# Optimization experiments

Hardware: AMD Instinct MI355X
Metric: run time of the kernel (lower is better)

The kernel has to match this reference:

```python
import jax, jax.numpy as jnp
import numpy as np

B, T, E, H = 4, 1024, 768, 12
HD = E // H                      # 64
R = 2                            # lora rank
LORA_SCALE = 1.0 / R             # loralib default lora_alpha=1 -> alpha/r
NUM_BUCKETS, MAX_DIST = 320, 800


def _rel_bucket(rel):
    nb = NUM_BUCKETS // 2                      # 160
    buckets = (rel > 0).astype(jnp.int32) * nb
    rel = jnp.abs(rel)
    max_exact = nb // 2                        # 80
    is_small = rel < max_exact
    log_ratio = jnp.log(jnp.maximum(rel, 1).astype(jnp.float32) / max_exact)
    large = max_exact + (log_ratio / np.log(MAX_DIST / max_exact) * (nb - max_exact)).astype(jnp.int32)
    large = jnp.minimum(large, nb - 1)
    return buckets + jnp.where(is_small, rel, large)


def setup_inputs() -> dict:
    key = jax.random.key(0)
    ks = jax.random.split(key, 22)
    s = 0.02
    w = lambda k, shape: jax.random.normal(k, shape, jnp.float32) * s
    return {
        "hidden_states": jax.random.normal(ks[0], (B, T, E), jnp.float32),
        "Wq": w(ks[1], (E, E)), "bq": w(ks[2], (E,)),
        "Wk": w(ks[3], (E, E)), "bk": w(ks[4], (E,)),
        "Wv": w(ks[5], (E, E)), "bv": w(ks[6], (E,)),
        "Aq": w(ks[7], (R, E)), "Bq": w(ks[8], (E, R)),
        "Ak": w(ks[9], (R, E)), "Bk": w(ks[10], (E, R)),
        "Av": w(ks[11], (R, E)), "Bv": w(ks[12], (E, R)),
        "Wo": w(ks[13], (E, E)), "bo": w(ks[14], (E,)),
        "Wg": w(ks[15], (8, HD)), "bg": w(ks[16], (8,)),
        "gru_const": jnp.ones((1, H, 1, 1), jnp.float32),
        "rel_embed": w(ks[17], (NUM_BUCKETS, H)),
    }


def reference(hidden_states, Wq, bq, Wk, bk, Wv, bv,
              Aq, Bq, Ak, Bk, Av, Bv, Wo, bo, Wg, bg, gru_const, rel_embed):
    Bsz, Tq, _ = hidden_states.shape
    # --- relative position bias [H, T, T] ---
    pos = jnp.arange(Tq)
    bucket = _rel_bucket(pos[None, :] - pos[:, None])
    pos_bias = rel_embed[bucket].transpose(2, 0, 1)
    # --- dynamic gate from hidden states, per head/position ---
    g = hidden_states.reshape(Bsz, Tq, H, HD).transpose(0, 2, 1, 3)      # [B,H,T,hd]
    gp = jnp.einsum('bhtd,ed->bhte', g, Wg) + bg                          # [B,H,T,8]
    gp = gp.reshape(Bsz, H, Tq, 2, 4).sum(-1)                             # [B,H,T,2]
    gates = jax.nn.sigmoid(gp)
    gate_a, gate_b = gates[..., :1], gates[..., 1:]
    gate = gate_a * (gate_b * gru_const - 1.0) + 2.0                      # [B,H,T,1]
    gated_bias = gate * pos_bias[None]                                    # [B,H,T,T]
    # --- projections: original double-applies q/k/v_proj (proj+LoRA, then
    #     again inside F.multi_head_attention_forward via separate proj weights) ---
    lin = lambda x, W, b: jnp.einsum('bte,oe->bto', x, W) + b
    lora = lambda x, A, Bm: jnp.einsum('bte,re,or->bto', x, A, Bm) * LORA_SCALE
    x = hidden_states
    q1 = lin(x, Wq, bq) + lora(x, Aq, Bq)
    k1 = lin(x, Wk, bk) + lora(x, Ak, Bk)
    v1 = lin(x, Wv, bv) + lora(x, Av, Bv)
    q = lin(q1, Wq, bq) * (HD ** -0.5)
    k = lin(k1, Wk, bk)
    v = lin(v1, Wv, bv)
    qh = q.reshape(Bsz, Tq, H, HD).transpose(0, 2, 1, 3)
    kh = k.reshape(Bsz, Tq, H, HD).transpose(0, 2, 1, 3)
    vh = v.reshape(Bsz, Tq, H, HD).transpose(0, 2, 1, 3)
    scores = jnp.einsum('bhqd,bhkd->bhqk', qh, kh) + gated_bias
    attn = jax.nn.softmax(scores, axis=-1)
    ctx = jnp.einsum('bhqk,bhkd->bhqd', attn, vh)
    out = ctx.transpose(0, 2, 1, 3).reshape(Bsz, Tq, E)
    return jnp.einsum('bte,oe->bto', out, Wo) + bo
```

## Files before the change

kernel.cpp:

```cpp
#include <hip/hip_runtime.h>
#include <math.h>

#define TT 1024
#define EE 768
#define HH 12

typedef __attribute__((ext_vector_type(8))) __bf16 bf16x8;
typedef __attribute__((ext_vector_type(4))) float f32x4;

__device__ __forceinline__ unsigned short f2b(float f) {
    unsigned int u = __float_as_uint(f);
    unsigned int r = (u + 0x7fffu + ((u >> 16) & 1u)) >> 16;
    return (unsigned short)r;
}

#define GLD16(gsrc, ldst) \
    __builtin_amdgcn_global_load_lds( \
        (const __attribute__((address_space(1))) unsigned int*)(gsrc), \
        (__attribute__((address_space(3))) unsigned int*)(ldst), 16, 0, 0)

__global__ __launch_bounds__(256)
void prep_k(const float* __restrict__ hs, const float* __restrict__ Wq,
            const float* __restrict__ Wk, const float* __restrict__ Wv,
            const float* __restrict__ Wo, unsigned short* __restrict__ out) {
    size_t i = 4 * (size_t)(blockIdx.x * 256 + threadIdx.x);
    if (i >= 5505024) return;
    const float* src;
    if (i < 3145728)      src = hs + i;
    else if (i < 3735552) src = Wq + (i - 3145728);
    else if (i < 4325376) src = Wk + (i - 3735552);
    else if (i < 4915200) src = Wv + (i - 4325376);
    else                  src = Wo + (i - 4915200);
    float4 f = *(const float4*)src;
    unsigned int lo = (unsigned int)f2b(f.x) | ((unsigned int)f2b(f.y) << 16);
    unsigned int hi = (unsigned int)f2b(f.z) | ((unsigned int)f2b(f.w) << 16);
    uint2 p; p.x = lo; p.y = hi;
    *(uint2*)&out[i] = p;
}

__global__ __launch_bounds__(256)
void wT_k(const float* __restrict__ Wq, const float* __restrict__ Wk,
          const float* __restrict__ Wv, unsigned short* __restrict__ WT_all) {
    __shared__ unsigned short Ts[128 * 136];
    const int v = blockIdx.x;
    const int mat = v / 36, tile = v % 36;
    const int tr = tile / 6, tc = tile % 6;
    const float* S = mat == 0 ? Wq : (mat == 1 ? Wk : Wv);
    const int tid = threadIdx.x;
    #pragma unroll
    for (int i = 0; i < 16; ++i) {
        int idx = i * 256 + tid;
        int row = idx >> 5, col4 = (idx & 31) * 4;
        float4 f = *(const float4*)&S[(size_t)(tr * 128 + row) * EE + tc * 128 + col4];
        Ts[(col4 + 0) * 136 + row] = f2b(f.x);
        Ts[(col4 + 1) * 136 + row] = f2b(f.y);
        Ts[(col4 + 2) * 136 + row] = f2b(f.z);
        Ts[(col4 + 3) * 136 + row] = f2b(f.w);
    }
    __syncthreads();
    unsigned short* dst = WT_all + (size_t)mat * 589824;
    #pragma unroll
    for (int i = 0; i < 8; ++i) {
        int idx = i * 256 + tid;
        int rr = idx >> 4, cg = (idx & 15) * 8;
        *(uint4*)&dst[(size_t)(tc * 128 + rr) * EE + tr * 128 + cg] =
            *(const uint4*)&Ts[rr * 136 + cg];
    }
}

__global__ void biastab_k(const float* __restrict__ rel_embed,
                          float* __restrict__ biasTab) {
    int idx = blockIdx.x * 256 + threadIdx.x;
    if (idx >= 2047 * 12) return;
    int h = idx % 12;
    int rr = idx / 12;
    int rel = rr - 1023;
    int base = rel > 0 ? 160 : 0;
    int ar = rel < 0 ? -rel : rel;
    int bkt;
    if (ar < 80) {
        bkt = base + ar;
    } else {
        double lr = log((double)ar / 80.0);
        int large = 80 + (int)(lr / log(10.0) * 80.0);
        if (large > 159) large = 159;
        bkt = base + large;
    }
    biasTab[h * 2048 + rr] = rel_embed[bkt * 12 + h];
}

__global__ __launch_bounds__(256)
void gates_k(const float* __restrict__ hs, const float* __restrict__ Wg,
             const float* __restrict__ bg, const float* __restrict__ gru,
             float* __restrict__ gate) {
    __shared__ float WgS[8][64];
    __shared__ float bgS[8];
    __shared__ float gcS[12];
    const int tid = threadIdx.x;
    for (int i = tid; i < 512; i += 256) WgS[i >> 6][i & 63] = Wg[i];
    if (tid < 8)  bgS[tid] = bg[tid];
    if (tid < 12) gcS[tid] = gru[tid];
    __syncthreads();
    int idx = blockIdx.x * 256 + tid;
    int t = idx & 1023;
    int h = (idx >> 10) % 12;
    int b = idx / (12 * 1024);
    const float* gp = hs + ((size_t)(b * TT + t)) * EE + h * 64;
    float acc[8];
    #pragma unroll
    for (int e = 0; e < 8; ++e) acc[e] = 0.f;
    #pragma unroll
    for (int d4 = 0; d4 < 64; d4 += 4) {
        float4 u = *(const float4*)(gp + d4);
        float gv[4] = {u.x, u.y, u.z, u.w};
        #pragma unroll
        for (int j = 0; j < 4; ++j) {
            #pragma unroll
            for (int e = 0; e < 8; ++e) acc[e] += gv[j] * WgS[e][d4 + j];
        }
    }
    float s0 = acc[0] + acc[1] + acc[2] + acc[3] + bgS[0] + bgS[1] + bgS[2] + bgS[3];
    float s1 = acc[4] + acc[5] + acc[6] + acc[7] + bgS[4] + bgS[5] + bgS[6] + bgS[7];
    float ga = 1.f / (1.f + __expf(-s0));
    float gb = 1.f / (1.f + __expf(-s1));
    gate[idx] = ga * (gb * gcS[h] - 1.0f) + 2.0f;
}

__global__ __launch_bounds__(64)
void lora_down_k(const float* __restrict__ x,
                 const float* __restrict__ Aq, const float* __restrict__ Ak,
                 const float* __restrict__ Av, float* __restrict__ xA) {
    const int m = blockIdx.x;
    const int lane = threadIdx.x;
    const float* xp = x + (size_t)m * EE;
    float s[6] = {0.f, 0.f, 0.f, 0.f, 0.f, 0.f};
    for (int c = lane * 4; c < EE; c += 256) {
        float4 u = *(const float4*)(xp + c);
        float xv[4] = {u.x, u.y, u.z, u.w};
        #pragma unroll
        for (int j = 0; j < 4; ++j) {
            int e = c + j;
            s[0] += xv[j] * Aq[e];       s[1] += xv[j] * Aq[EE + e];
            s[2] += xv[j] * Ak[e];       s[3] += xv[j] * Ak[EE + e];
            s[4] += xv[j] * Av[e];       s[5] += xv[j] * Av[EE + e];
        }
    }
    #pragma unroll
    for (int off = 32; off > 0; off >>= 1) {
        #pragma unroll
        for (int i = 0; i < 6; ++i) s[i] += __shfl_down(s[i], off, 64);
    }
    if (lane == 0) {
        xA[m * 2 + 0] = s[0];                xA[m * 2 + 1] = s[1];
        xA[8192 + m * 2 + 0] = s[2];         xA[8192 + m * 2 + 1] = s[3];
        xA[16384 + m * 2 + 0] = s[4];        xA[16384 + m * 2 + 1] = s[5];
    }
}

__global__ __launch_bounds__(256)
void bias2_k(const float* __restrict__ Wq, const float* __restrict__ Wk,
             const float* __restrict__ Wv,
             const float* __restrict__ bq, const float* __restrict__ bk,
             const float* __restrict__ bv,
             const float* __restrict__ Bq, const float* __restrict__ Bk,
             const float* __restrict__ Bv,
             float* __restrict__ bias2, float* __restrict__ B2) {
    __shared__ float bvS[768];
    __shared__ float BmS[1536];
    const int tid = threadIdx.x;
    int v = blockIdx.x;
    int sel = v / 4, nb = (v % 4) * 192;
    const float* W = sel == 0 ? Wq : (sel == 1 ? Wk : Wv);
    const float* bvec = sel == 0 ? bq : (sel == 1 ? bk : bv);
    const float* Bm = sel == 0 ? Bq : (sel == 1 ? Bk : Bv);
    for (int i = tid; i < 768; i += 256) bvS[i] = bvec[i];
    for (int i = tid; i < 1536; i += 256) BmS[i] = Bm[i];
    __syncthreads();
    if (tid < 192) {
        int n = nb + tid;
        const float* Wrow = W + (size_t)n * EE;
        float a0 = 0.f, a1 = 0.f, a2 = 0.f;
        for (int o = 0; o < EE; o += 4) {
            float4 w = *(const float4*)&Wrow[o];
            a0 += w.x * bvS[o] + w.y * bvS[o + 1] + w.z * bvS[o + 2] + w.w * bvS[o + 3];
            a1 += w.x * BmS[o * 2] + w.y * BmS[o * 2 + 2] + w.z * BmS[o * 2 + 4] + w.w * BmS[o * 2 + 6];
            a2 += w.x * BmS[o * 2 + 1] + w.y * BmS[o * 2 + 3] + w.z * BmS[o * 2 + 5] + w.w * BmS[o * 2 + 7];
        }
        bias2[sel * 768 + n] = a0 + bvS[n];
        B2[sel * 1536 + n * 2 + 0] = a1;
        B2[sel * 1536 + n * 2 + 1] = a2;
    }
}

__global__ __launch_bounds__(256, 2)
void wgemm_k(const unsigned short* __restrict__ Wall_b,
             const unsigned short* __restrict__ WT_all,
             unsigned short* __restrict__ W2_all) {
    __shared__ unsigned short At[128 * 32];
    __shared__ unsigned short Bt[128 * 32];
    const int tid = threadIdx.x;
    const int bxx = blockIdx.x;
    const int sel = bxx / 36, tile = bxx % 36;
    const int row0 = (tile / 6) * 128, col0 = (tile % 6) * 128;
    const unsigned short* A = Wall_b + (size_t)sel * 589824;
    const unsigned short* Bw = WT_all + (size_t)sel * 589824;

    const int lane = tid & 63, wv = tid >> 6;
    const int wm = (wv & 1) * 64, wn = (wv >> 1) * 64;
    const int l15 = lane & 15, g8 = (lane >> 4) * 8;
    const int lr = lane >> 2, lc = (lane & 3) * 8;
    const int c0 = wv * 2, c1 = wv * 2 + 1;
    const unsigned short* Abase0 = A + (size_t)(row0 + c0 * 16 + lr) * EE + lc;
    const unsigned short* Abase1 = A + (size_t)(row0 + c1 * 16 + lr) * EE + lc;
    const unsigned short* Bbase0 = Bw + (size_t)(col0 + c0 * 16 + lr) * EE + lc;
    const unsigned short* Bbase1 = Bw + (size_t)(col0 + c1 * 16 + lr) * EE + lc;

    f32x4 zero4 = {0.f, 0.f, 0.f, 0.f};
    f32x4 acc[4][4];
    #pragma unroll
    for (int i = 0; i < 4; ++i)
        #pragma unroll
        for (int j = 0; j < 4; ++j) acc[i][j] = zero4;

    for (int kt = 0; kt < 768; kt += 32) {
        GLD16(Abase0 + kt, &At[c0 * 512]);
        GLD16(Abase1 + kt, &At[c1 * 512]);
        GLD16(Bbase0 + kt, &Bt[c0 * 512]);
        GLD16(Bbase1 + kt, &Bt[c1 * 512]);
        __syncthreads();
        bf16x8 af[4], bf[4];
        #pragma unroll
        for (int mt = 0; mt < 4; ++mt) af[mt] = *(const bf16x8*)&At[(wm + mt * 16 + l15) * 32 + g8];
        #pragma unroll
        for (int nt = 0; nt < 4; ++nt) bf[nt] = *(const bf16x8*)&Bt[(wn + nt * 16 + l15) * 32 + g8];
        #pragma unroll
        for (int mt = 0; mt < 4; ++mt)
            #pragma unroll
            for (int nt = 0; nt < 4; ++nt)
                acc[mt][nt] = __builtin_amdgcn_mfma_f32_16x16x32_bf16(af[mt], bf[nt], acc[mt][nt], 0, 0, 0);
        __syncthreads();
    }
    unsigned short* out = W2_all + (size_t)sel * 589824;
    const int g4 = (lane >> 4) * 4;
    #pragma unroll
    for (int mt = 0; mt < 4; ++mt)
        #pragma unroll
        for (int r = 0; r < 4; ++r) {
            int grow = row0 + wm + mt * 16 + g4 + r;
            #pragma unroll
            for (int nt = 0; nt < 4; ++nt) {
                int ncol = col0 + wn + nt * 16 + l15;
                out[(size_t)grow * EE + ncol] = f2b(acc[mt][nt][r]);
            }
        }
}

__global__ __launch_bounds__(256, 2)
void qkv_gemm_k(const unsigned short* __restrict__ Aall,
                const unsigned short* __restrict__ W2_all,
                const float* __restrict__ bias2,
                const float* __restrict__ xA, const float* __restrict__ B2,
                unsigned short* __restrict__ qb, unsigned short* __restrict__ kb,
                unsigned short* __restrict__ vb) {
    __shared__ unsigned short At[128 * 32];
    __shared__ unsigned short Bt[128 * 32];
    const int tid = threadIdx.x;
    const int bx = blockIdx.x, by = blockIdx.y;
    const int sel = bx / 6;
    const int col0 = (bx % 6) * 128, row0 = by * 128;
    const unsigned short* Wb = W2_all + (size_t)sel * 589824;
    const float* bias = bias2 + sel * 768;
    const float scale = (sel == 0) ? 0.125f : 1.0f;

    const int lane = tid & 63, wv = tid >> 6;
    const int wm = (wv & 1) * 64, wn = (wv >> 1) * 64;
    const int l15 = lane & 15, g8 = (lane >> 4) * 8;
    const int lr = lane >> 2, lc = (lane & 3) * 8;
    const int c0 = wv * 2, c1 = wv * 2 + 1;
    const unsigned short* Abase0 = Aall + (size_t)(row0 + c0 * 16 + lr) * EE + lc;
    const unsigned short* Abase1 = Aall + (size_t)(row0 + c1 * 16 + lr) * EE + lc;
    const unsigned short* Bbase0 = Wb + (size_t)(col0 + c0 * 16 + lr) * EE + lc;
    const unsigned short* Bbase1 = Wb + (size_t)(col0 + c1 * 16 + lr) * EE + lc;

    f32x4 zero4 = {0.f, 0.f, 0.f, 0.f};
    f32x4 acc[4][4];
    #pragma unroll
    for (int i = 0; i < 4; ++i)
        #pragma unroll
        for (int j = 0; j < 4; ++j) acc[i][j] = zero4;

    for (int kt = 0; kt < 768; kt += 32) {
        GLD16(Abase0 + kt, &At[c0 * 512]);
        GLD16(Abase1 + kt, &At[c1 * 512]);
        GLD16(Bbase0 + kt, &Bt[c0 * 512]);
        GLD16(Bbase1 + kt, &Bt[c1 * 512]);
        __syncthreads();
        bf16x8 af[4], bf[4];
        #pragma unroll
        for (int mt = 0; mt < 4; ++mt) af[mt] = *(const bf16x8*)&At[(wm + mt * 16 + l15) * 32 + g8];
        #pragma unroll
        for (int nt = 0; nt < 4; ++nt) bf[nt] = *(const bf16x8*)&Bt[(wn + nt * 16 + l15) * 32 + g8];
        #pragma unroll
        for (int mt = 0; mt < 4; ++mt)
            #pragma unroll
            for (int nt = 0; nt < 4; ++nt)
                acc[mt][nt] = __builtin_amdgcn_mfma_f32_16x16x32_bf16(af[mt], bf[nt], acc[mt][nt], 0, 0, 0);
        __syncthreads();
    }

    unsigned short* dst = sel == 0 ? qb : (sel == 1 ? kb : vb);
    const float* Lbase = xA + sel * 8192;
    const float* B2s   = B2 + sel * 1536;
    const int g4 = (lane >> 4) * 4;
    #pragma unroll
    for (int mt = 0; mt < 4; ++mt) {
        #pragma unroll
        for (int r = 0; r < 4; ++r) {
            size_t grow = (size_t)row0 + wm + mt * 16 + g4 + r;
            float l0 = Lbase[grow * 2], l1 = Lbase[grow * 2 + 1];
            #pragma unroll
            for (int nt = 0; nt < 4; ++nt) {
                int ncol = col0 + wn + nt * 16 + l15;
                float c = (acc[mt][nt][r] + bias[ncol]
                           + 0.5f * (l0 * B2s[ncol * 2] + l1 * B2s[ncol * 2 + 1])) * scale;
                dst[grow * EE + ncol] = f2b(c);
            }
        }
    }
}

__global__ __launch_bounds__(256)
void vT_k(const unsigned short* __restrict__ vb, unsigned short* __restrict__ Vtg) {
    __shared__ unsigned short Vs[64 * 72];
    const int tid = threadIdx.x;
    const int tt = blockIdx.x, h = blockIdx.y, b = blockIdx.z;
    const int r = tid >> 3, cc = (tid & 7) * 8;
    #pragma unroll
    for (int i = 0; i < 2; ++i) {
        int row = i * 32 + r;
        const unsigned short* vp = vb + (size_t)(b * TT + tt * 64 + row) * EE + h * 64 + cc;
        *(uint4*)&Vs[row * 72 + cc] = *(const uint4*)vp;
    }
    __syncthreads();
    #pragma unroll
    for (int i = 0; i < 2; ++i) {
        int d = i * 32 + r;
        unsigned short tmp[8] __attribute__((aligned(16)));
        #pragma unroll
        for (int j = 0; j < 8; ++j) tmp[j] = Vs[(cc + j) * 72 + d];
        *(uint4*)&Vtg[((size_t)(b * HH + h) * 64 + d) * TT + tt * 64 + cc] = *(const uint4*)tmp;
    }
}

__global__ __launch_bounds__(256, 3)
void attn_k(const unsigned short* __restrict__ qb, const unsigned short* __restrict__ kb,
            const unsigned short* __restrict__ Vtg, const float* __restrict__ gate,
            const float* __restrict__ biasTab, unsigned short* __restrict__ ctx) {
    __shared__ unsigned short Qs[64 * 72];
    __shared__ unsigned short Ks[64 * 72];
    __shared__ unsigned short Vt[64 * 72];
    __shared__ unsigned short Ps[64 * 72];
    __shared__ float btabS[2048];
    const int tid = threadIdx.x;
    const int qt = blockIdx.x, h = blockIdx.y, b = blockIdx.z;

    for (int i = tid; i < 2047; i += 256) btabS[i] = biasTab[h * 2048 + i];

    const int srow = tid >> 2, scol = (tid & 3) * 16;
    {
        const unsigned short* qp = qb + ((size_t)(b * TT + qt * 64 + srow)) * EE + h * 64 + scol;
        *(uint4*)&Qs[srow * 72 + scol]     = *(const uint4*)qp;
        *(uint4*)&Qs[srow * 72 + scol + 8] = *(const uint4*)(qp + 8);
    }
    const int lane = tid & 63, wv = tid >> 6;
    const int m0 = wv * 16;
    const int l15 = lane & 15, g = lane >> 4;

    float li[4];
    f32x4 zero4 = {0.f, 0.f, 0.f, 0.f};
    f32x4 oa[4];
    #pragma unroll
    for (int r = 0; r < 4; ++r) li[r] = 0.f;
    #pragma unroll
    for (int nt = 0; nt < 4; ++nt) oa[nt] = zero4;
    float gv[4];
    #pragma unroll
    for (int r = 0; r < 4; ++r)
        gv[r] = gate[((size_t)(b * HH + h)) * TT + qt * 64 + m0 + 4 * g + r];
    const unsigned short* vrow = Vtg + ((size_t)(b * HH + h) * 64 + srow) * TT;
    __syncthreads();

    for (int kt = 0; kt < 16; ++kt) {
        {
            const unsigned short* kp = kb + ((size_t)(b * TT + kt * 64 + srow)) * EE + h * 64 + scol;
            *(uint4*)&Ks[srow * 72 + scol]     = *(const uint4*)kp;
            *(uint4*)&Ks[srow * 72 + scol + 8] = *(const uint4*)(kp + 8);
            const unsigned short* vp = vrow + kt * 64 + scol;
            *(uint4*)&Vt[srow * 72 + scol]     = *(const uint4*)vp;
            *(uint4*)&Vt[srow * 72 + scol + 8] = *(const uint4*)(vp + 8);
        }
        __syncthreads();
        f32x4 sa[4];
        #pragma unroll
        for (int nt = 0; nt < 4; ++nt) sa[nt] = zero4;
        bf16x8 aq0 = *(const bf16x8*)&Qs[(m0 + l15) * 72 + g * 8];
        bf16x8 aq1 = *(const bf16x8*)&Qs[(m0 + l15) * 72 + 32 + g * 8];
        #pragma unroll
        for (int nt = 0; nt < 4; ++nt) {
            bf16x8 bk0 = *(const bf16x8*)&Ks[(nt * 16 + l15) * 72 + g * 8];
            bf16x8 bk1 = *(const bf16x8*)&Ks[(nt * 16 + l15) * 72 + 32 + g * 8];
            sa[nt] = __builtin_amdgcn_mfma_f32_16x16x32_bf16(aq0, bk0, sa[nt], 0, 0, 0);
            sa[nt] = __builtin_amdgcn_mfma_f32_16x16x32_bf16(aq1, bk1, sa[nt], 0, 0, 0);
        }
        #pragma unroll
        for (int nt = 0; nt < 4; ++nt) {
            int ibase = kt * 64 + nt * 16 + l15 + 1023 - qt * 64 - m0 - 4 * g;
            #pragma unroll
            for (int r = 0; r < 4; ++r) {
                float e = __expf(sa[nt][r] + gv[r] * btabS[ibase - r]);
                li[r] += e;
                Ps[(m0 + 4 * g + r) * 72 + nt * 16 + l15] = f2b(e);
            }
        }
        bf16x8 ap0 = *(const bf16x8*)&Ps[(m0 + l15) * 72 + g * 8];
        bf16x8 ap1 = *(const bf16x8*)&Ps[(m0 + l15) * 72 + 32 + g * 8];
        #pragma unroll
        for (int nt = 0; nt < 4; ++nt) {
            bf16x8 bv0 = *(const bf16x8*)&Vt[(nt * 16 + l15) * 72 + g * 8];
            bf16x8 bv1 = *(const bf16x8*)&Vt[(nt * 16 + l15) * 72 + 32 + g * 8];
            oa[nt] = __builtin_amdgcn_mfma_f32_16x16x32_bf16(ap0, bv0, oa[nt], 0, 0, 0);
            oa[nt] = __builtin_amdgcn_mfma_f32_16x16x32_bf16(ap1, bv1, oa[nt], 0, 0, 0);
        }
        __syncthreads();
    }
    #pragma unroll
    for (int r = 0; r < 4; ++r) {
        #pragma unroll
        for (int msk = 1; msk < 16; msk <<= 1)
            li[r] += __shfl_xor(li[r], msk, 16);
    }
    #pragma unroll
    for (int nt = 0; nt < 4; ++nt)
        #pragma unroll
        for (int r = 0; r < 4; ++r)
            Ks[(m0 + 4 * g + r) * 72 + nt * 16 + l15] = f2b(oa[nt][r] / li[r]);
    __syncthreads();
    {
        unsigned short* cp = ctx + ((size_t)(b * TT + qt * 64 + srow)) * EE + h * 64 + scol;
        *(uint4*)cp       = *(const uint4*)&Ks[srow * 72 + scol];
        *(uint4*)(cp + 8) = *(const uint4*)&Ks[srow * 72 + scol + 8];
    }
}

__global__ __launch_bounds__(256, 2)
void out_gemm_k(const unsigned short* __restrict__ Aall,
                const unsigned short* __restrict__ Wob,
                const float* __restrict__ bo, float* __restrict__ outf) {
    __shared__ unsigned short At[128 * 32];
    __shared__ unsigned short Bt[128 * 32];
    const int tid = threadIdx.x;
    const int col0 = blockIdx.x * 128, row0 = blockIdx.y * 128;

    const int lane = tid & 63, wv = tid >> 6;
    const int wm = (wv & 1) * 64, wn = (wv >> 1) * 64;
    const int l15 = lane & 15, g8 = (lane >> 4) * 8;
    const int lr = lane >> 2, lc = (lane & 3) * 8;
    const int c0 = wv * 2, c1 = wv * 2 + 1;
    const unsigned short* Abase0 = Aall + (size_t)(row0 + c0 * 16 + lr) * EE + lc;
    const unsigned short* Abase1 = Aall + (size_t)(row0 + c1 * 16 + lr) * EE + lc;
    const unsigned short* Bbase0 = Wob + (size_t)(col0 + c0 * 16 + lr) * EE + lc;
    const unsigned short* Bbase1 = Wob + (size_t)(col0 + c1 * 16 + lr) * EE + lc;

    f32x4 zero4 = {0.f, 0.f, 0.f, 0.f};
    f32x4 acc[4][4];
    #pragma unroll
    for (int i = 0; i < 4; ++i)
        #pragma unroll
        for (int j = 0; j < 4; ++j) acc[i][j] = zero4;

    for (int kt = 0; kt < 768; kt += 32) {
        GLD16(Abase0 + kt, &At[c0 * 512]);
        GLD16(Abase1 + kt, &At[c1 * 512]);
        GLD16(Bbase0 + kt, &Bt[c0 * 512]);
        GLD16(Bbase1 + kt, &Bt[c1 * 512]);
        __syncthreads();
        bf16x8 af[4], bf[4];
        #pragma unroll
        for (int mt = 0; mt < 4; ++mt) af[mt] = *(const bf16x8*)&At[(wm + mt * 16 + l15) * 32 + g8];
        #pragma unroll
        for (int nt = 0; nt < 4; ++nt) bf[nt] = *(const bf16x8*)&Bt[(wn + nt * 16 + l15) * 32 + g8];
        #pragma unroll
        for (int mt = 0; mt < 4; ++mt)
            #pragma unroll
            for (int nt = 0; nt < 4; ++nt)
                acc[mt][nt] = __builtin_amdgcn_mfma_f32_16x16x32_bf16(af[mt], bf[nt], acc[mt][nt], 0, 0, 0);
        __syncthreads();
    }
    const int g4 = (lane >> 4) * 4;
    #pragma unroll
    for (int mt = 0; mt < 4; ++mt)
        #pragma unroll
        for (int r = 0; r < 4; ++r) {
            size_t grow = (size_t)row0 + wm + mt * 16 + g4 + r;
            #pragma unroll
            for (int nt = 0; nt < 4; ++nt) {
                int ncol = col0 + wn + nt * 16 + l15;
                outf[grow * EE + ncol] = acc[mt][nt][r] + bo[ncol];
            }
        }
}

extern "C" void kernel_launch(void* const* d_in, const int* in_sizes, int n_in,
                              void* d_out, int out_size, void* d_ws, size_t ws_size,
                              hipStream_t stream) {
    const float* hs  = (const float*)d_in[0];
    const float* Wq  = (const float*)d_in[1];
    const float* bq  = (const float*)d_in[2];
    const float* Wk  = (const float*)d_in[3];
    const float* bk  = (const float*)d_in[4];
    const float* Wv  = (const float*)d_in[5];
    const float* bv  = (const float*)d_in[6];
    const float* Aq  = (const float*)d_in[7];
    const float* Bq  = (const float*)d_in[8];
    const float* Ak  = (const float*)d_in[9];
    const float* Bk  = (const float*)d_in[10];
    const float* Av  = (const float*)d_in[11];
    const float* Bv  = (const float*)d_in[12];
    const float* Wo  = (const float*)d_in[13];
    const float* bo  = (const float*)d_in[14];
    const float* Wg  = (const float*)d_in[15];
    const float* bg  = (const float*)d_in[16];
    const float* gru = (const float*)d_in[17];
    const float* rel = (const float*)d_in[18];

    float* ws = (float*)d_ws;
    float* gate    = ws;
    float* biasTab = gate + 49152;
    float* xA      = biasTab + 24576;
    float* bias2   = xA + 24576;
    float* B2      = bias2 + 2304;
    unsigned short* hsb    = (unsigned short*)(B2 + 4608);
    unsigned short* Wall_b = hsb + 3145728;
    unsigned short* WT_all = Wall_b + 4 * 589824;
    unsigned short* W2_all = WT_all + 3 * 589824;
    unsigned short* qb     = W2_all + 3 * 589824;
    unsigned short* kb     = qb + 3145728;
    unsigned short* vb     = kb + 3145728;
    unsigned short* Vtg    = vb + 3145728;
    unsigned short* ctxb   = Vtg + 3145728;

    prep_k<<<5376, 256, 0, stream>>>(hs, Wq, Wk, Wv, Wo, hsb);
    wT_k<<<108, 256, 0, stream>>>(Wq, Wk, Wv, WT_all);
    gates_k<<<192, 256, 0, stream>>>(hs, Wg, bg, gru, gate);
    lora_down_k<<<4096, 64, 0, stream>>>(hs, Aq, Ak, Av, xA);
    biastab_k<<<96, 256, 0, stream>>>(rel, biasTab);
    bias2_k<<<12, 256, 0, stream>>>(Wq, Wk, Wv, bq, bk, bv, Bq, Bk, Bv, bias2, B2);

    wgemm_k<<<108, 256, 0, stream>>>(Wall_b, WT_all, W2_all);
    qkv_gemm_k<<<dim3(18, 32), 256, 0, stream>>>(hsb, W2_all, bias2, xA, B2, qb, kb, vb);
    vT_k<<<dim3(16, 12, 4), 256, 0, stream>>>(vb, Vtg);
    attn_k<<<dim3(16, 12, 4), 256, 0, stream>>>(qb, kb, Vtg, gate, biasTab, ctxb);
    out_gemm_k<<<dim3(6, 32), 256, 0, stream>>>(ctxb, Wall_b + 3 * 589824, bo, (float*)d_out);
}
```

Measured before the change: 260.6 us.

## Merge setup kernels, fuse hs reads, prefetch K/V in attention, raise occupancy

Six preprocessing launches become two. One block-partitioned kernel handles weight casts, the W transpose, the bias table and bias2. The other reads each 16-row slab of hidden states once to produce the bf16 copy, the gates and the LoRA down-projection. The q scale of 0.125 moves from the qkv GEMM epilogue into W2 and bias2. The attention kernel now prefetches the next K/V tile into registers while the current tile is computed, and the GEMM launch bounds change from 2 to 3 blocks per SM. This cuts launch overhead and redundant hs traffic, at the cost of more register pressure and a possible drop in occupancy in the fused kernels.

```diff
diff --git a/kernel.cpp b/kernel.cpp
--- a/kernel.cpp
+++ b/kernel.cpp
@@ -20,179 +20,196 @@
         (__attribute__((address_space(3))) unsigned int*)(ldst), 16, 0, 0)
 
 __global__ __launch_bounds__(256)
-void prep_k(const float* __restrict__ hs, const float* __restrict__ Wq,
-            const float* __restrict__ Wk, const float* __restrict__ Wv,
-            const float* __restrict__ Wo, unsigned short* __restrict__ out) {
-    size_t i = 4 * (size_t)(blockIdx.x * 256 + threadIdx.x);
-    if (i >= 5505024) return;
-    const float* src;
-    if (i < 3145728)      src = hs + i;
-    else if (i < 3735552) src = Wq + (i - 3145728);
-    else if (i < 4325376) src = Wk + (i - 3735552);
-    else if (i < 4915200) src = Wv + (i - 4325376);
-    else                  src = Wo + (i - 4915200);
-    float4 f = *(const float4*)src;
-    unsigned int lo = (unsigned int)f2b(f.x) | ((unsigned int)f2b(f.y) << 16);
-    unsigned int hi = (unsigned int)f2b(f.z) | ((unsigned int)f2b(f.w) << 16);
-    uint2 p; p.x = lo; p.y = hi;
-    *(uint2*)&out[i] = p;
+void setupA_k(const float* __restrict__ Wq, const float* __restrict__ Wk,
+              const float* __restrict__ Wv, const float* __restrict__ Wo,
+              const float* __restrict__ bq, const float* __restrict__ bk,
+              const float* __restrict__ bv,
+              const float* __restrict__ Bq, const float* __restrict__ Bk,
+              const float* __restrict__ Bv, const float* __restrict__ rel,
+              unsigned short* __restrict__ Wall_b, unsigned short* __restrict__ WT_all,
+              float* __restrict__ biasTab, float* __restrict__ bias2,
+              float* __restrict__ B2) {
+    __shared__ __align__(16) char smem[34816];
+    const int bid = blockIdx.x, tid = threadIdx.x;
+
+    if (bid < 1152) {
+        size_t base = (size_t)bid * 2048 + tid * 8;
+        int mat = (int)(base / 589824);
+        size_t local = base % 589824;
+        const float* S = mat == 0 ? Wq : (mat == 1 ? Wk : (mat == 2 ? Wv : Wo));
+        float4 a = *(const float4*)&S[local];
+        float4 c = *(const float4*)&S[local + 4];
+        unsigned short hb[8] __attribute__((aligned(16)));
+        hb[0] = f2b(a.x); hb[1] = f2b(a.y); hb[2] = f2b(a.z); hb[3] = f2b(a.w);
+        hb[4] = f2b(c.x); hb[5] = f2b(c.y); hb[6] = f2b(c.z); hb[7] = f2b(c.w);
+        *(uint4*)&Wall_b[base] = *(const uint4*)hb;
+    } else if (bid < 1260) {
+        unsigned short* Ts = (unsigned short*)smem;
+        int v = bid - 1152;
+        int mat = v / 36, tile = v % 36;
+        int tr = tile / 6, tc = tile % 6;
+        const float* S = mat == 0 ? Wq : (mat == 1 ? Wk : Wv);
+        #pragma unroll
+        for (int i = 0; i < 16; ++i) {
+            int idx = i * 256 + tid;
+            int row = idx >> 5, col4 = (idx & 31) * 4;
+            float4 f = *(const float4*)&S[(size_t)(tr * 128 + row) * EE + tc * 128 + col4];
+            Ts[(col4 + 0) * 136 + row] = f2b(f.x);
+            Ts[(col4 + 1) * 136 + row] = f2b(f.y);
+            Ts[(col4 + 2) * 136 + row] = f2b(f.z);
+            Ts[(col4 + 3) * 136 + row] = f2b(f.w);
+        }
+        __syncthreads();
+        unsigned short* dst = WT_all + (size_t)mat * 589824;
+        #pragma unroll
+        for (int i = 0; i < 8; ++i) {
+            int idx = i * 256 + tid;
+            int rr = idx >> 4, cg = (idx & 15) * 8;
+            *(uint4*)&dst[(size_t)(tc * 128 + rr) * EE + tr * 128 + cg] =
+                *(const uint4*)&Ts[rr * 136 + cg];
+        }
+    } else if (bid < 1356) {
+        int idx = (bid - 1260) * 256 + tid;
+        if (idx < 2047 * 12) {
+            int h = idx % 12;
+            int rr = idx / 12;
+            int relv = rr - 1023;
+            int base = relv > 0 ? 160 : 0;
+            int ar = relv < 0 ? -relv : relv;
+            int bkt;
+            if (ar < 80) bkt = base + ar;
+            else {
+                double lr = log((double)ar / 80.0);
+                int large = 80 + (int)(lr / log(10.0) * 80.0);
+                if (large > 159) large = 159;
+                bkt = base + large;
+            }
+            biasTab[h * 2048 + rr] = rel[bkt * 12 + h];
+        }
+    } else {
+        float* bvS = (float*)smem;
+        float* BmS = bvS + 768;
+        int v = bid - 1356;
+        int sel = v / 4, nb = (v % 4) * 192;
+        const float* W = sel == 0 ? Wq : (sel == 1 ? Wk : Wv);
+        const float* bvec = sel == 0 ? bq : (sel == 1 ? bk : bv);
+        const float* Bm = sel == 0 ? Bq : (sel == 1 ? Bk : Bv);
+        for (int i = tid; i < 768; i += 256) bvS[i] = bvec[i];
+        for (int i = tid; i < 1536; i += 256) BmS[i] = Bm[i];
+        __syncthreads();
+        if (tid < 192) {
+            int n = nb + tid;
+            const float* Wrow = W + (size_t)n * EE;
+            float a0 = 0.f, a1 = 0.f, a2 = 0.f;
+            for (int o = 0; o < EE; o += 4) {
+                float4 w = *(const float4*)&Wrow[o];
+                a0 += w.x * bvS[o] + w.y * bvS[o + 1] + w.z * bvS[o + 2] + w.w * bvS[o + 3];
+                a1 += w.x * BmS[o * 2] + w.y * BmS[o * 2 + 2] + w.z * BmS[o * 2 + 4] + w.w * BmS[o * 2 + 6];
+                a2 += w.x * BmS[o * 2 + 1] + w.y * BmS[o * 2 + 3] + w.z * BmS[o * 2 + 5] + w.w * BmS[o * 2 + 7];
+            }
+            float sc = (sel == 0) ? 0.125f : 1.0f;
+            bias2[sel * 768 + n] = (a0 + bvS[n]) * sc;
+            B2[sel * 1536 + n * 2 + 0] = a1 * sc;
+            B2[sel * 1536 + n * 2 + 1] = a2 * sc;
+        }
+    }
 }
 
 __global__ __launch_bounds__(256)
-void wT_k(const float* __restrict__ Wq, const float* __restrict__ Wk,
-          const float* __restrict__ Wv, unsigned short* __restrict__ WT_all) {
-    __shared__ unsigned short Ts[128 * 136];
-    const int v = blockIdx.x;
-    const int mat = v / 36, tile = v % 36;
-    const int tr = tile / 6, tc = tile % 6;
-    const float* S = mat == 0 ? Wq : (mat == 1 ? Wk : Wv);
-    const int tid = threadIdx.x;
-    #pragma unroll
-    for (int i = 0; i < 16; ++i) {
-        int idx = i * 256 + tid;
-        int row = idx >> 5, col4 = (idx & 31) * 4;
-        float4 f = *(const float4*)&S[(size_t)(tr * 128 + row) * EE + tc * 128 + col4];
-        Ts[(col4 + 0) * 136 + row] = f2b(f.x);
-        Ts[(col4 + 1) * 136 + row] = f2b(f.y);
-        Ts[(col4 + 2) * 136 + row] = f2b(f.z);
-        Ts[(col4 + 3) * 136 + row] = f2b(f.w);
-    }
-    __syncthreads();
-    unsigned short* dst = WT_all + (size_t)mat * 589824;
-    #pragma unroll
-    for (int i = 0; i < 8; ++i) {
-        int idx = i * 256 + tid;
-        int rr = idx >> 4, cg = (idx & 15) * 8;
-        *(uint4*)&dst[(size_t)(tc * 128 + rr) * EE + tr * 128 + cg] =
-            *(const uint4*)&Ts[rr * 136 + cg];
-    }
-}
-
-__global__ void biastab_k(const float* __restrict__ rel_embed,
-                          float* __restrict__ biasTab) {
-    int idx = blockIdx.x * 256 + threadIdx.x;
-    if (idx >= 2047 * 12) return;
-    int h = idx % 12;
-    int rr = idx / 12;
-    int rel = rr - 1023;
-    int base = rel > 0 ? 160 : 0;
-    int ar = rel < 0 ? -rel : rel;
-    int bkt;
-    if (ar < 80) {
-        bkt = base + ar;
-    } else {
-        double lr = log((double)ar / 80.0);
-        int large = 80 + (int)(lr / log(10.0) * 80.0);
-        if (large > 159) large = 159;
-        bkt = base + large;
-    }
-    biasTab[h * 2048 + rr] = rel_embed[bkt * 12 + h];
-}
-
-__global__ __launch_bounds__(256)
-void gates_k(const float* __restrict__ hs, const float* __restrict__ Wg,
-             const float* __restrict__ bg, const float* __restrict__ gru,
-             float* __restrict__ gate) {
-    __shared__ float WgS[8][64];
+void setupB_k(const float* __restrict__ hs, const float* __restrict__ Wg,
+              const float* __restrict__ bg, const float* __restrict__ gru,
+              const float* __restrict__ Aq, const float* __restrict__ Ak,
+              const float* __restrict__ Av,
+              unsigned short* __restrict__ hsb, float* __restrict__ gate,
+              float* __restrict__ xA) {
+    __shared__ float rowF[16 * 772];
+    __shared__ float AS[6 * 768];
+    __shared__ float WgS[8 * 68];
+    __shared__ float gpS[16 * 100];
+    __shared__ float redS[4 * 96];
     __shared__ float bgS[8];
     __shared__ float gcS[12];
     const int tid = threadIdx.x;
-    for (int i = tid; i < 512; i += 256) WgS[i >> 6][i & 63] = Wg[i];
+    const int m0 = blockIdx.x * 16;
+
+    for (int i = tid; i < 512; i += 256) WgS[(i >> 6) * 68 + (i & 63)] = Wg[i];
+    for (int i = tid; i < 1152; i += 256) {
+        int which = i / 192, c4 = (i % 192) * 4;
+        const float* src = (which < 2 ? Aq : (which < 4 ? Ak : Av)) + (which & 1) * 768 + c4;
+        float4 f = *(const float4*)src;
+        AS[which * 768 + c4 + 0] = f.x; AS[which * 768 + c4 + 1] = f.y;
+        AS[which * 768 + c4 + 2] = f.z; AS[which * 768 + c4 + 3] = f.w;
+    }
     if (tid < 8)  bgS[tid] = bg[tid];
     if (tid < 12) gcS[tid] = gru[tid];
+    #pragma unroll
+    for (int i = 0; i < 12; ++i) {
+        int idx = i * 256 + tid;
+        int row = idx / 192, c4 = (idx % 192) * 4;
+        float4 f = *(const float4*)&hs[(size_t)(m0 + row) * EE + c4];
+        rowF[row * 772 + c4 + 0] = f.x; rowF[row * 772 + c4 + 1] = f.y;
+        rowF[row * 772 + c4 + 2] = f.z; rowF[row * 772 + c4 + 3] = f.w;
+        unsigned int lo = (unsigned int)f2b(f.x) | ((unsigned int)f2b(f.y) << 16);
+        unsigned int hi = (unsigned int)f2b(f.z) | ((unsigned int)f2b(f.w) << 16);
+        uint2 p; p.x = lo; p.y = hi;
+        *(uint2*)&hsb[(size_t)(m0 + row) * EE + c4] = p;
+    }
     __syncthreads();
-    int idx = blockIdx.x * 256 + tid;
-    int t = idx & 1023;
-    int h = (idx >> 10) % 12;
-    int b = idx / (12 * 1024);
-    const float* gp = hs + ((size_t)(b * TT + t)) * EE + h * 64;
-    float acc[8];
-    #pragma unroll
-    for (int e = 0; e < 8; ++e) acc[e] = 0.f;
-    #pragma unroll
-    for (int d4 = 0; d4 < 64; d4 += 4) {
-        float4 u = *(const float4*)(gp + d4);
-        float gv[4] = {u.x, u.y, u.z, u.w};
-        #pragma unroll
-        for (int j = 0; j < 4; ++j) {
-            #pragma unroll
-            for (int e = 0; e < 8; ++e) acc[e] += gv[j] * WgS[e][d4 + j];
-        }
-    }
-    float s0 = acc[0] + acc[1] + acc[2] + acc[3] + bgS[0] + bgS[1] + bgS[2] + bgS[3];
-    float s1 = acc[4] + acc[5] + acc[6] + acc[7] + bgS[4] + bgS[5] + bgS[6] + bgS[7];
-    float ga = 1.f / (1.f + __expf(-s0));
-    float gb = 1.f / (1.f + __expf(-s1));
-    gate[idx] = ga * (gb * gcS[h] - 1.0f) + 2.0f;
-}
-
-__global__ __launch_bounds__(64)
-void lora_down_k(const float* __restrict__ x,
-                 const float* __restrict__ Aq, const float* __restrict__ Ak,
-                 const float* __restrict__ Av, float* __restrict__ xA) {
-    const int m = blockIdx.x;
-    const int lane = threadIdx.x;
-    const float* xp = x + (size_t)m * EE;
-    float s[6] = {0.f, 0.f, 0.f, 0.f, 0.f, 0.f};
-    for (int c = lane * 4; c < EE; c += 256) {
-        float4 u = *(const float4*)(xp + c);
-        float xv[4] = {u.x, u.y, u.z, u.w};
-        #pragma unroll
-        for (int j = 0; j < 4; ++j) {
-            int e = c + j;
-            s[0] += xv[j] * Aq[e];       s[1] += xv[j] * Aq[EE + e];
-            s[2] += xv[j] * Ak[e];       s[3] += xv[j] * Ak[EE + e];
-            s[4] += xv[j] * Av[e];       s[5] += xv[j] * Av[EE + e];
-        }
-    }
-    #pragma unroll
-    for (int off = 32; off > 0; off >>= 1) {
-        #pragma unroll
-        for (int i = 0; i < 6; ++i) s[i] += __shfl_down(s[i], off, 64);
-    }
-    if (lane == 0) {
-        xA[m * 2 + 0] = s[0];                xA[m * 2 + 1] = s[1];
-        xA[8192 + m * 2 + 0] = s[2];         xA[8192 + m * 2 + 1] = s[3];
-        xA[16384 + m * 2 + 0] = s[4];        xA[16384 + m * 2 + 1] = s[5];
-    }
-}
-
-__global__ __launch_bounds__(256)
-void bias2_k(const float* __restrict__ Wq, const float* __restrict__ Wk,
-             const float* __restrict__ Wv,
-             const float* __restrict__ bq, const float* __restrict__ bk,
-             const float* __restrict__ bv,
-             const float* __restrict__ Bq, const float* __restrict__ Bk,
-             const float* __restrict__ Bv,
-             float* __restrict__ bias2, float* __restrict__ B2) {
-    __shared__ float bvS[768];
-    __shared__ float BmS[1536];
-    const int tid = threadIdx.x;
-    int v = blockIdx.x;
-    int sel = v / 4, nb = (v % 4) * 192;
-    const float* W = sel == 0 ? Wq : (sel == 1 ? Wk : Wv);
-    const float* bvec = sel == 0 ? bq : (sel == 1 ? bk : bv);
-    const float* Bm = sel == 0 ? Bq : (sel == 1 ? Bk : Bv);
-    for (int i = tid; i < 768; i += 256) bvS[i] = bvec[i];
-    for (int i = tid; i < 1536; i += 256) BmS[i] = Bm[i];
+    #pragma unroll
+    for (int j = 0; j < 6; ++j) {
+        int idx = j * 256 + tid;
+        int row = idx & 15, q = idx >> 4;
+        int h = q % 12, e = q / 12;
+        const float* rp = &rowF[row * 772 + h * 64];
+        const float* wp = &WgS[e * 68];
+        float a = 0.f;
+        #pragma unroll 16
+        for (int d = 0; d < 64; ++d) a += rp[d] * wp[d];
+        gpS[row * 100 + h * 8 + e] = a;
+    }
+    {
+        int row = tid & 15, seg = tid >> 4;
+        float s[6] = {0.f, 0.f, 0.f, 0.f, 0.f, 0.f};
+        #pragma unroll 8
+        for (int j = 0; j < 48; ++j) {
+            int e = seg * 48 + j;
+            float xv = rowF[row * 772 + e];
+            s[0] += xv * AS[e];            s[1] += xv * AS[768 + e];
+            s[2] += xv * AS[1536 + e];     s[3] += xv * AS[2304 + e];
+            s[4] += xv * AS[3072 + e];     s[5] += xv * AS[3840 + e];
+        }
+        #pragma unroll
+        for (int i = 0; i < 6; ++i) {
+            s[i] += __shfl_xor(s[i], 16, 64);
+            s[i] += __shfl_xor(s[i], 32, 64);
+        }
+        int lane = tid & 63, w = tid >> 6;
+        if ((lane >> 4) == 0)
+            #pragma unroll
+            for (int i = 0; i < 6; ++i) redS[w * 96 + row * 6 + i] = s[i];
+    }
     __syncthreads();
+    if (tid < 96) {
+        int row = tid / 6, i = tid % 6;
+        float v = redS[row * 6 + i] + redS[96 + row * 6 + i] +
+                  redS[192 + row * 6 + i] + redS[288 + row * 6 + i];
+        int sel = i >> 1, r = i & 1;
+        xA[sel * 8192 + (size_t)(m0 + row) * 2 + r] = v;
+    }
     if (tid < 192) {
-        int n = nb + tid;
-        const float* Wrow = W + (size_t)n * EE;
-        float a0 = 0.f, a1 = 0.f, a2 = 0.f;
-        for (int o = 0; o < EE; o += 4) {
-            float4 w = *(const float4*)&Wrow[o];
-            a0 += w.x * bvS[o] + w.y * bvS[o + 1] + w.z * bvS[o + 2] + w.w * bvS[o + 3];
-            a1 += w.x * BmS[o * 2] + w.y * BmS[o * 2 + 2] + w.z * BmS[o * 2 + 4] + w.w * BmS[o * 2 + 6];
-            a2 += w.x * BmS[o * 2 + 1] + w.y * BmS[o * 2 + 3] + w.z * BmS[o * 2 + 5] + w.w * BmS[o * 2 + 7];
-        }
-        bias2[sel * 768 + n] = a0 + bvS[n];
-        B2[sel * 1536 + n * 2 + 0] = a1;
-        B2[sel * 1536 + n * 2 + 1] = a2;
-    }
-}
-
-__global__ __launch_bounds__(256, 2)
+        int row = tid / 12, h = tid % 12;
+        const float* gp = &gpS[row * 100 + h * 8];
+        float s0 = gp[0] + gp[1] + gp[2] + gp[3] + bgS[0] + bgS[1] + bgS[2] + bgS[3];
+        float s1 = gp[4] + gp[5] + gp[6] + gp[7] + bgS[4] + bgS[5] + bgS[6] + bgS[7];
+        float ga = 1.f / (1.f + __expf(-s0));
+        float gb = 1.f / (1.f + __expf(-s1));
+        int m = m0 + row;
+        int b = m >> 10, tp = m & 1023;
+        gate[((size_t)b * HH + h) * TT + tp] = ga * (gb * gcS[h] - 1.0f) + 2.0f;
+    }
+}
+
+__global__ __launch_bounds__(256, 3)
 void wgemm_k(const unsigned short* __restrict__ Wall_b,
              const unsigned short* __restrict__ WT_all,
              unsigned short* __restrict__ W2_all) {
@@ -241,6 +258,7 @@
         __syncthreads();
     }
     unsigned short* out = W2_all + (size_t)sel * 589824;
+    const float sc = (sel == 0) ? 0.125f : 1.0f;
     const int g4 = (lane >> 4) * 4;
     #pragma unroll
     for (int mt = 0; mt < 4; ++mt)
@@ -250,12 +268,12 @@
             #pragma unroll
             for (int nt = 0; nt < 4; ++nt) {
                 int ncol = col0 + wn + nt * 16 + l15;
-                out[(size_t)grow * EE + ncol] = f2b(acc[mt][nt][r]);
+                out[(size_t)grow * EE + ncol] = f2b(acc[mt][nt][r] * sc);
             }
         }
 }
 
-__global__ __launch_bounds__(256, 2)
+__global__ __launch_bounds__(256, 3)
 void qkv_gemm_k(const unsigned short* __restrict__ Aall,
                 const unsigned short* __restrict__ W2_all,
                 const float* __restrict__ bias2,
@@ -270,7 +288,6 @@
     const int col0 = (bx % 6) * 128, row0 = by * 128;
     const unsigned short* Wb = W2_all + (size_t)sel * 589824;
     const float* bias = bias2 + sel * 768;
-    const float scale = (sel == 0) ? 0.125f : 1.0f;
 
     const int lane = tid & 63, wv = tid >> 6;
     const int wm = (wv & 1) * 64, wn = (wv >> 1) * 64;
@@ -321,8 +338,8 @@
             #pragma unroll
             for (int nt = 0; nt < 4; ++nt) {
                 int ncol = col0 + wn + nt * 16 + l15;
-                float c = (acc[mt][nt][r] + bias[ncol]
-                           + 0.5f * (l0 * B2s[ncol * 2] + l1 * B2s[ncol * 2 + 1])) * scale;
+                float c = acc[mt][nt][r] + bias[ncol]
+                          + 0.5f * (l0 * B2s[ncol * 2] + l1 * B2s[ncol * 2 + 1]);
                 dst[grow * EE + ncol] = f2b(c);
             }
         }
@@ -387,19 +404,30 @@
     #pragma unroll
     for (int r = 0; r < 4; ++r)
         gv[r] = gate[((size_t)(b * HH + h)) * TT + qt * 64 + m0 + 4 * g + r];
-    const unsigned short* vrow = Vtg + ((size_t)(b * HH + h) * 64 + srow) * TT;
-    __syncthreads();
+
+    const unsigned short* kpbase = kb + ((size_t)(b * TT + srow)) * EE + h * 64 + scol;
+    const unsigned short* vpbase = Vtg + ((size_t)(b * HH + h) * 64 + srow) * TT + scol;
+
+    uint4 kr0 = *(const uint4*)kpbase;
+    uint4 kr1 = *(const uint4*)(kpbase + 8);
+    uint4 vr0 = *(const uint4*)vpbase;
+    uint4 vr1 = *(const uint4*)(vpbase + 8);
 
     for (int kt = 0; kt < 16; ++kt) {
-        {
-            const unsigned short* kp = kb + ((size_t)(b * TT + kt * 64 + srow)) * EE + h * 64 + scol;
-            *(uint4*)&Ks[srow * 72 + scol]     = *(const uint4*)kp;
-            *(uint4*)&Ks[srow * 72 + scol + 8] = *(const uint4*)(kp + 8);
-            const unsigned short* vp = vrow + kt * 64 + scol;
-            *(uint4*)&Vt[srow * 72 + scol]     = *(const uint4*)vp;
-            *(uint4*)&Vt[srow * 72 + scol + 8] = *(const uint4*)(vp + 8);
-        }
-        __syncthreads();
+        __syncthreads();
+        *(uint4*)&Ks[srow * 72 + scol]     = kr0;
+        *(uint4*)&Ks[srow * 72 + scol + 8] = kr1;
+        *(uint4*)&Vt[srow * 72 + scol]     = vr0;
+        *(uint4*)&Vt[srow * 72 + scol + 8] = vr1;
+        __syncthreads();
+        if (kt < 15) {
+            const unsigned short* kp = kpbase + (size_t)(kt + 1) * 64 * EE;
+            kr0 = *(const uint4*)kp;
+            kr1 = *(const uint4*)(kp + 8);
+            const unsigned short* vp = vpbase + (kt + 1) * 64;
+            vr0 = *(const uint4*)vp;
+            vr1 = *(const uint4*)(vp + 8);
+        }
         f32x4 sa[4];
         #pragma unroll
         for (int nt = 0; nt < 4; ++nt) sa[nt] = zero4;
@@ -431,8 +459,8 @@
             oa[nt] = __builtin_amdgcn_mfma_f32_16x16x32_bf16(ap0, bv0, oa[nt], 0, 0, 0);
             oa[nt] = __builtin_amdgcn_mfma_f32_16x16x32_bf16(ap1, bv1, oa[nt], 0, 0, 0);
         }
-        __syncthreads();
-    }
+    }
+    __syncthreads();
     #pragma unroll
     for (int r = 0; r < 4; ++r) {
         #pragma unroll
@@ -452,7 +480,7 @@
     }
 }
 
-__global__ __launch_bounds__(256, 2)
+__global__ __launch_bounds__(256, 3)
 void out_gemm_k(const unsigned short* __restrict__ Aall,
                 const unsigned short* __restrict__ Wob,
                 const float* __restrict__ bo, float* __restrict__ outf) {
@@ -549,13 +577,9 @@
     unsigned short* Vtg    = vb + 3145728;
     unsigned short* ctxb   = Vtg + 3145728;
 
-    prep_k<<<5376, 256, 0, stream>>>(hs, Wq, Wk, Wv, Wo, hsb);
-    wT_k<<<108, 256, 0, stream>>>(Wq, Wk, Wv, WT_all);
-    gates_k<<<192, 256, 0, stream>>>(hs, Wg, bg, gru, gate);
-    lora_down_k<<<4096, 64, 0, stream>>>(hs, Aq, Ak, Av, xA);
-    biastab_k<<<96, 256, 0, stream>>>(rel, biasTab);
-    bias2_k<<<12, 256, 0, stream>>>(Wq, Wk, Wv, bq, bk, bv, Bq, Bk, Bv, bias2, B2);
-
+    setupA_k<<<1368, 256, 0, stream>>>(Wq, Wk, Wv, Wo, bq, bk, bv, Bq, Bk, Bv, rel,
+                                       Wall_b, WT_all, biasTab, bias2, B2);
+    setupB_k<<<256, 256, 0, stream>>>(hs, Wg, bg, gru, Aq, Ak, Av, hsb, gate, xA);
     wgemm_k<<<108, 256, 0, stream>>>(Wall_b, WT_all, W2_all);
     qkv_gemm_k<<<dim3(18, 32), 256, 0, stream>>>(hsb, W2_all, bias2, xA, B2, qb, kb, vb);
     vT_k<<<dim3(16, 12, 4), 256, 0, stream>>>(vb, Vtg);
```

After: 248.3 us. -4.7%, faster.
